# Kernel optimization log

Measured on AMD Instinct MI355X. Metric: run time of the kernel, lower is better.

The kernel has to match this reference:

```python
import jax, jax.numpy as jnp
import numpy as np
from jax import lax

STRIDE, HID, LAT, R, LVL, SCALE = 8, 128, 64, 3, 4, 4
FF = 50 * 60  # frame_flow spatial size


def bilinear_sample(img, x, y):
    # img: [Q,C,H,W]; x,y: [Q,P] float pixel coords; zero outside image. -> [Q,C,P]
    Q, C, H, W = img.shape
    x0 = jnp.floor(x); y0 = jnp.floor(y)
    wx = x - x0; wy = y - y0
    flat = img.reshape(Q, C, H * W)
    def g(ix, iy):
        valid = (ix >= 0) & (ix <= W - 1) & (iy >= 0) & (iy <= H - 1)
        idx = (jnp.clip(iy, 0, H - 1).astype(jnp.int32) * W
               + jnp.clip(ix, 0, W - 1).astype(jnp.int32))[:, None, :]
        v = jnp.take_along_axis(flat, jnp.broadcast_to(idx, (Q, C, x.shape[-1])), axis=2)
        return v * valid[:, None, :]
    return (g(x0, y0) * ((1 - wy) * (1 - wx))[:, None, :]
            + g(x0 + 1, y0) * ((1 - wy) * wx)[:, None, :]
            + g(x0, y0 + 1) * (wy * (1 - wx))[:, None, :]
            + g(x0 + 1, y0 + 1) * (wy * wx)[:, None, :])


def resize_bilinear(img, oh, ow, align_corners):
    # img: [Q,C,H,W] -> [Q,C,oh,ow], matches F.interpolate(mode='bilinear')
    Q, C, H, W = img.shape
    def coords(o, i):
        if align_corners:
            return jnp.linspace(0.0, i - 1.0, o)
        return jnp.clip((jnp.arange(o) + 0.5) * (i / o) - 0.5, 0.0, i - 1.0)
    ys, xs = coords(oh, H), coords(ow, W)
    y0 = jnp.floor(ys).astype(jnp.int32); y1 = jnp.minimum(y0 + 1, H - 1); wy = ys - y0
    x0 = jnp.floor(xs).astype(jnp.int32); x1 = jnp.minimum(x0 + 1, W - 1); wx = xs - x0
    v = jnp.take(img, y0, axis=2) * (1 - wy)[:, None] + jnp.take(img, y1, axis=2) * wy[:, None]
    return jnp.take(v, x0, axis=3) * (1 - wx) + jnp.take(v, x1, axis=3) * wx


def avg_pool2(x):
    return lax.reduce_window(x, 0.0, lax.add, (1, 1, 2, 2), (1, 1, 2, 2), 'VALID') * 0.25


def encode(x, w, stride):
    # patchify conv + instance-norm (surrogate for BasicEncoder, same in/out shapes)
    y = lax.conv_general_dilated(x, w, (stride, stride), 'VALID',
                                 dimension_numbers=('NCHW', 'OIHW', 'NCHW'))
    m = y.mean(axis=(2, 3), keepdims=True)
    v = y.var(axis=(2, 3), keepdims=True)
    return (y - m) * lax.rsqrt(v + 1e-5)


def build_pyramid(fmaps):
    # fmaps: [B,S,C,H,W] -> list of [B*S,C,Hl,Wl] (CorrBlock.__init__)
    B, S, C, H, W = fmaps.shape
    x = fmaps.reshape(B * S, C, H, W)
    pyr = [x]
    for _ in range(LVL - 1):
        x = avg_pool2(x)
        pyr.append(x)
    return pyr


def corr_pyramid(pyr, feats):
    # feats: [B,S,N,C] -> list of [B*S,N,Hl,Wl] (CorrBlock.corr)
    B, S, N, C = feats.shape
    f = feats.reshape(B * S, N, C)
    scale = 1.0 / jnp.sqrt(jnp.float32(C))
    return [jnp.einsum('qnc,qchw->qnhw', f, p) * scale for p in pyr]


def corr_sample(corrs, coords):
    # CorrBlock.sample: bilinear gather of (2R+1)^2 window per level at coords/2^lvl
    B, S, N, _ = coords.shape
    d = jnp.arange(-R, R + 1, dtype=coords.dtype)
    dy, dx = jnp.meshgrid(d, d, indexing='ij')
    dx = dx.reshape(1, -1); dy = dy.reshape(1, -1)
    out = []
    for i, c in enumerate(corrs):
        H, W = c.shape[-2:]
        cen = coords.reshape(B * S * N, 1, 2) / (2.0 ** i)
        x = cen[..., 0] + dx; y = cen[..., 1] + dy  # [BSN,K]
        v = bilinear_sample(c.reshape(B * S * N, 1, H, W), x, y)
        out.append(v.reshape(B, S, N, -1))
    return jnp.concatenate(out, axis=-1)  # [B,S,N,LVL*(2R+1)^2]


def flows_from(coords):
    B, S, N, _ = coords.shape
    f = (coords[:, 1:] - coords[:, :-1]).transpose(0, 2, 1, 3).reshape(B * N, S - 1, 2)
    return jnp.concatenate([f, f[:, -1:]], axis=1)


def delta_block(fc, fl, ff, xy, w1, b1, w2, b2):
    # surrogate for DeltaBlock / DeltaBlock_temp: MLP over concatenated context
    h = jnp.concatenate([fc, fl, ff, xy], axis=-1)
    return jax.nn.relu(h @ w1 + b1) @ w2 + b2  # [B*N,S,2]


def forward_model(rgbs, points_0, fnet_w, fnet_fine_w, linear_w, linear_b,
                  dbs_w1, dbs_b1, dbs_w2, dbs_b2,
                  dbt_w1, dbt_b1, dbt_w2, dbt_b2, iters):
    B, S, C, H, W = rgbs.shape
    N = points_0.shape[1]
    rgbs = 2.0 * (rgbs / 255.0) - 1.0
    rgbs_ = rgbs.reshape(B * S, C, H, W)
    # frame_flow context (assumes B==1, like the torch code): [N,S,3000]
    ff = jnp.concatenate([rgbs_[-1:, 0], rgbs_[1:, 0] - rgbs_[:-1, 0]], axis=0)[:, None]
    ff = resize_bilinear(ff, 50, 60, False).reshape(1, S, FF)
    frame_flow = jnp.broadcast_to(ff, (N, S, FF))

    # ---- initialize_ : coarse stage (stride 8) ----
    Hc, Wc = H // STRIDE, W // STRIDE
    fmaps_c = encode(rgbs_, fnet_w, STRIDE).reshape(B, S, LAT, Hc, Wc)
    coords = jnp.broadcast_to((points_0 / float(STRIDE))[:, None], (B, S, N, 2))
    f0 = bilinear_sample(fmaps_c[:, 0], coords[:, 0, :, 0], coords[:, 0, :, 1]).transpose(0, 2, 1)
    feats = jnp.broadcast_to(f0[:, None], (B, S, N, LAT))
    xys0_c = jnp.broadcast_to(coords[:, 0].transpose(1, 0, 2), (N, S, 2))
    coords = lax.stop_gradient(coords)
    corrs_c = corr_pyramid(build_pyramid(fmaps_c), feats)
    fc = [resize_bilinear(c, 14, 14, True).reshape(B, S, N, 196) for c in corrs_c]
    fcorrs_ = jnp.stack(fc).mean(0).transpose(0, 2, 1, 3).reshape(B * N, S, 196)
    delta = delta_block(fcorrs_, flows_from(coords), frame_flow, xys0_c,
                        dbs_w1, dbs_b1, dbs_w2, dbs_b2)
    coords = coords + delta.reshape(B, N, S, 2).transpose(0, 2, 1, 3)
    coords_init = coords * float(STRIDE)

    # ---- fine refinement (stride 2), iterative ----
    fs = STRIDE // SCALE  # 2
    Hf, Wf = H // fs, W // fs
    fmaps = encode(rgbs_, fnet_fine_w, fs).reshape(B, S, LAT, Hf, Wf)
    coords = coords_init / float(fs)
    pyr = build_pyramid(fmaps)
    f0 = bilinear_sample(fmaps[:, 0], coords[:, 0, :, 0], coords[:, 0, :, 1]).transpose(0, 2, 1)
    corrs1 = corr_pyramid(pyr, jnp.broadcast_to(f0[:, None], (B, S, N, LAT)))
    xys0 = jnp.broadcast_to(coords[:, 0].transpose(1, 0, 2), (N, S, 2))
    inds2 = jnp.clip(jnp.arange(S) - 2, 0, None)
    inds4 = jnp.clip(jnp.arange(S) - 4, 0, None)
    preds = [coords_init]
    for _ in range(iters):
        coords = lax.stop_gradient(coords)
        def shifted_feats(inds, coords=coords):
            fm = fmaps[:, inds].reshape(B * S, LAT, Hf, Wf)
            co = coords[:, inds].reshape(B * S, N, 2)
            return bilinear_sample(fm, co[..., 0], co[..., 1]).transpose(0, 2, 1).reshape(B, S, N, LAT)
        corrs2 = corr_pyramid(pyr, shifted_feats(inds2))
        corrs4 = corr_pyramid(pyr, shifted_feats(inds4))
        def bn(f):
            return f.transpose(0, 2, 1, 3).reshape(B * N, S, -1)
        fcorrs_ = jnp.concatenate([bn(corr_sample(corrs1, coords)),
                                   bn(corr_sample(corrs2, coords)),
                                   bn(corr_sample(corrs4, coords))], axis=2)
        fcorrs_ = fcorrs_ @ linear_w + linear_b  # 588 -> 392
        delta = delta_block(fcorrs_, flows_from(coords), frame_flow, xys0,
                            dbt_w1, dbt_b1, dbt_w2, dbt_b2)
        coords = coords + delta.reshape(B, N, S, 2).transpose(0, 2, 1, 3)
        preds.append(coords * float(fs))
    return jnp.stack(preds)  # [iters+1, B, S, N, 2]


def setup_inputs():
    ks = jax.random.split(jax.random.key(0), 12)
    B, S, N, H, W = 1, 16, 64, 200, 240
    rgbs = jax.random.uniform(ks[0], (B, S, 1, H, W), jnp.float32) * 255.0
    points_0 = jax.random.uniform(ks[1], (B, N, 2), jnp.float32) * jnp.array([W - 1.0, H - 1.0], jnp.float32)
    d_sp, d_tp = 196 + 2 + FF + 2, 392 + 2 + FF + 2
    return {
        'rgbs': rgbs, 'points_0': points_0,
        'fnet_w': jax.random.normal(ks[2], (LAT, 1, STRIDE, STRIDE), jnp.float32) * 0.1,
        'fnet_fine_w': jax.random.normal(ks[3], (LAT, 1, 2, 2), jnp.float32) * 0.3,
        'linear_w': jax.random.normal(ks[4], (588, 392), jnp.float32) / np.sqrt(588.0).astype(np.float32),
        'linear_b': jnp.zeros((392,), jnp.float32),
        'dbs_w1': jax.random.normal(ks[5], (d_sp, HID), jnp.float32) / np.float32(np.sqrt(d_sp)),
        'dbs_b1': jnp.zeros((HID,), jnp.float32),
        'dbs_w2': jax.random.normal(ks[6], (HID, 2), jnp.float32) / np.float32(np.sqrt(HID)),
        'dbs_b2': jnp.zeros((2,), jnp.float32),
        'dbt_w1': jax.random.normal(ks[7], (d_tp, HID), jnp.float32) / np.float32(np.sqrt(d_tp)),
        'dbt_b1': jnp.zeros((HID,), jnp.float32),
        'dbt_w2': jax.random.normal(ks[8], (HID, 2), jnp.float32) / np.float32(np.sqrt(HID)),
        'dbt_b2': jnp.zeros((2,), jnp.float32),
        'iters': 4,
    }


def reference(rgbs, points_0, fnet_w, fnet_fine_w, linear_w, linear_b,
              dbs_w1, dbs_b1, dbs_w2, dbs_b2,
              dbt_w1, dbt_b1, dbt_w2, dbt_b2, iters):
    return forward_model(rgbs, points_0, fnet_w, fnet_fine_w, linear_w, linear_b,
                         dbs_w1, dbs_b1, dbs_w2, dbs_b2,
                         dbt_w1, dbt_b1, dbt_w2, dbt_b2, iters)
```

## Files before the change

kernel.cpp:

```cpp
#include <hip/hip_runtime.h>

constexpr int cS = 16, cN = 64, cH = 200, cW = 240;
constexpr int cHC = 25, cWC = 30;
constexpr int cHF = 100, cWF = 120;
constexpr int cC = 64;
constexpr int cITERS = 4;
constexpr int cNCH = 50, cCHUNK = 60;

typedef _Float16 half8 __attribute__((ext_vector_type(8)));
typedef _Float16 h2 __attribute__((ext_vector_type(2)));


__device__ __forceinline__ float bilin_raw_h(const _Float16* __restrict__ fm, int Hh, int Ww,
                                             float x, float y, int c, float& wsum) {
  x = fminf(fmaxf(x, -2.0e6f), 2.0e6f);
  y = fminf(fmaxf(y, -2.0e6f), 2.0e6f);
  float x0f = floorf(x), y0f = floorf(y);
  int ix = (int)x0f, iy = (int)y0f;
  float wx = x - x0f, wy = y - y0f;
  float acc = 0.f; wsum = 0.f;
  bool vx0 = (ix >= 0) && (ix < Ww), vx1 = (ix + 1 >= 0) && (ix + 1 < Ww);
  bool vy0 = (iy >= 0) && (iy < Hh), vy1 = (iy + 1 >= 0) && (iy + 1 < Hh);
  float w00 = (1.f - wy) * (1.f - wx), w01 = (1.f - wy) * wx;
  float w10 = wy * (1.f - wx), w11 = wy * wx;
  if (vy0 && vx0) { acc += (float)fm[(iy * Ww + ix) * cC + c] * w00; wsum += w00; }
  if (vy0 && vx1) { acc += (float)fm[(iy * Ww + ix + 1) * cC + c] * w01; wsum += w01; }
  if (vy1 && vx0) { acc += (float)fm[((iy + 1) * Ww + ix) * cC + c] * w10; wsum += w10; }
  if (vy1 && vx1) { acc += (float)fm[((iy + 1) * Ww + ix + 1) * cC + c] * w11; wsum += w11; }
  return acc;
}

constexpr int NB_FFP = 800, NB_CONVC = 400, NB_CONVF = 1600;

__global__ __launch_bounds__(256) void k_front(const float* __restrict__ rgbs,
                                               const float* __restrict__ w1s,
                                               const float* __restrict__ w1t,
                                               const float* __restrict__ fnw,
                                               const float* __restrict__ fnfw,
                                               float* __restrict__ part,
                                               _Float16* __restrict__ fmc,
                                               float* __restrict__ partc,
                                               _Float16* __restrict__ fmf,
                                               float* __restrict__ partf) {
  __shared__ float smem[6528];
  int bid = blockIdx.x, tid = threadIdx.x;
  const float a = 2.0f / 255.0f;

  if (bid < NB_FFP) {
    int s = bid / cNCH, ch = bid % cNCH;
    if (tid < cCHUNK) {
      const float* cur = rgbs + (size_t)s * cH * cW;
      const float* prev = rgbs + (size_t)(s - 1) * cH * cW;
      const float* last = rgbs + (size_t)15 * cH * cW;
      int y = 4 * ch + 1, x = 4 * tid + 1;
      float v = 0.f;
      #pragma unroll
      for (int dy = 0; dy < 2; dy++)
        #pragma unroll
        for (int dx = 0; dx < 2; dx++) {
          int id = (y + dy) * cW + (x + dx);
          float pv = (s == 0) ? (a * last[id] - 1.0f) : (a * (cur[id] - prev[id]));
          v += pv;
        }
      smem[tid] = 0.25f * v;
    }
    __syncthreads();
    int t = tid >> 7, j = tid & 127;
    const float* w = (t == 0) ? (w1s + (size_t)198 * 128) : (w1t + (size_t)394 * 128);
    const float* wr = w + (size_t)ch * cCHUNK * 128 + j;
    float acc = 0.f;
    #pragma unroll 4
    for (int i = 0; i < cCHUNK; i++) acc += smem[i] * wr[(size_t)i * 128];
    part[(((size_t)t * cS + s) * cNCH + ch) * 128 + j] = acc;

  } else if (bid < NB_FFP + NB_CONVC) {
    int idx = bid - NB_FFP;
    int q = idx / 25, y = idx % 25;
    float* imgL = smem;
    float* wlT = smem + 1920;
    float* red = smem + 6016;
    const float* img = rgbs + ((size_t)q * cH + y * 8) * cW;
    for (int i = tid; i < 1920; i += 256) imgL[i] = img[i];
    for (int i = tid; i < 4096; i += 256) {
      int tap = i >> 6, c = i & 63;
      wlT[i] = fnw[c * 64 + tap];
    }
    __syncthreads();
    int c = tid & 63, g = tid >> 6;
    float wsum = 0.f;
    for (int t = 0; t < 64; t++) wsum += wlT[t * 64 + c];
    float sum = 0.f, ss = 0.f;
    for (int x = g; x < 30; x += 4) {
      float acc = 0.f;
      #pragma unroll
      for (int ky = 0; ky < 8; ky++)
        #pragma unroll
        for (int kx = 0; kx < 8; kx++)
          acc += wlT[(ky * 8 + kx) * 64 + c] * imgL[ky * 240 + x * 8 + kx];
      float v = a * acc - wsum;
      fmc[((size_t)q * 750 + y * 30 + x) * cC + c] = (_Float16)v;
      sum += v; ss += v * v;
    }
    red[(0 * 4 + g) * 64 + c] = sum;
    red[(1 * 4 + g) * 64 + c] = ss;
    __syncthreads();
    if (g == 0) {
      float s4 = red[0 * 64 + c] + red[1 * 64 + c] + red[2 * 64 + c] + red[3 * 64 + c];
      float q4 = red[(4 + 0) * 64 + c] + red[(4 + 1) * 64 + c] +
                 red[(4 + 2) * 64 + c] + red[(4 + 3) * 64 + c];
      size_t o = ((size_t)q * 25 + y) * 64 + c;
      partc[o * 2 + 0] = s4;
      partc[o * 2 + 1] = q4;
    }

  } else {
    int idx = bid - NB_FFP - NB_CONVC;
    int q = idx / cHF, y = idx % cHF;
    int lane = tid & 63, wv = tid >> 6;
    float w0 = fnfw[lane * 4 + 0], w1 = fnfw[lane * 4 + 1];
    float w2 = fnfw[lane * 4 + 2], w3 = fnfw[lane * 4 + 3];
    float wsum = w0 + w1 + w2 + w3;
    const float* img = rgbs + (size_t)q * cH * cW;
    float sum = 0.f, ss = 0.f;
    for (int x = wv; x < cWF; x += 4) {
      const float* b = img + (2 * y) * cW + 2 * x;
      float v = a * (w0 * b[0] + w1 * b[1] + w2 * b[cW] + w3 * b[cW + 1]) - wsum;
      fmf[(((size_t)q * cHF + y) * cWF + x) * cC + lane] = (_Float16)v;
      sum += v; ss += v * v;
    }
    float* red = smem;
    red[(0 * 4 + wv) * 64 + lane] = sum;
    red[(1 * 4 + wv) * 64 + lane] = ss;
    __syncthreads();
    if (wv == 0) {
      float s4 = red[0 * 64 + lane] + red[1 * 64 + lane] + red[2 * 64 + lane] + red[3 * 64 + lane];
      float q4 = red[(4 + 0) * 64 + lane] + red[(4 + 1) * 64 + lane] +
                 red[(4 + 2) * 64 + lane] + red[(4 + 3) * 64 + lane];
      size_t o = ((size_t)q * cHF + y) * 64 + lane;
      partf[o * 2 + 0] = s4;
      partf[o * 2 + 1] = q4;
    }
  }
}

__global__ __launch_bounds__(256) void k_mid(const float* __restrict__ part,
                                             float* __restrict__ ffw_s, float* __restrict__ ffw_t,
                                             const float* __restrict__ lw, const float* __restrict__ lb,
                                             const float* __restrict__ w1t, const float* __restrict__ b1t,
                                             h2* __restrict__ LWc2, float* __restrict__ b1te,
                                             const float* __restrict__ partf, float* __restrict__ stats,
                                             const float* __restrict__ partc, float* __restrict__ statc,
                                             const _Float16* __restrict__ fmc, float* __restrict__ arp) {
  __shared__ float smem[14784];
  int bid = blockIdx.x, tid = threadIdx.x;

  if (bid < 16) {
    int s = bid, t = tid >> 7, j = tid & 127;
    const float* p = part + (((size_t)t * cS + s) * cNCH) * 128 + j;
    float acc = 0.f;
    for (int c = 0; c < cNCH; c++) acc += p[(size_t)c * 128];
    ((t == 0) ? ffw_s : ffw_t)[s * 128 + j] = acc;

  } else if (bid < 91) {
    int b2 = bid - 16, g = tid >> 7, j = tid & 127;
    if (b2 < 74) {
      int k0 = b2 * 8 + g * 4;
      if (k0 < 588) {
        const float* l0 = lw + (size_t)(k0 + 0) * 392;
        const float* l1 = lw + (size_t)(k0 + 1) * 392;
        const float* l2 = lw + (size_t)(k0 + 2) * 392;
        const float* l3 = lw + (size_t)(k0 + 3) * 392;
        float a0 = 0.f, a1 = 0.f, a2 = 0.f, a3 = 0.f;
        for (int m = 0; m < 392; m++) {
          float wv = w1t[(size_t)m * 128 + j];
          a0 += l0[m] * wv; a1 += l1[m] * wv; a2 += l2[m] * wv; a3 += l3[m] * wv;
        }
        int kk = k0 >> 1;
        LWc2[(size_t)(kk + 0) * 128 + j] = h2{(_Float16)a0, (_Float16)a1};
        LWc2[(size_t)(kk + 1) * 128 + j] = h2{(_Float16)a2, (_Float16)a3};
      }
    } else if (g == 0) {
      float acc = b1t[j];
      for (int m = 0; m < 392; m++) acc += lb[m] * w1t[(size_t)m * 128 + j];
      b1te[j] = acc;
    }

  } else if (bid < 107) {
    int q = bid - 91, c = tid & 63, g = tid >> 6;
    float s0 = 0.f, s1 = 0.f;
    for (int yy = 0; yy < 25; yy++) {
      size_t o = ((size_t)q * cHF + g * 25 + yy) * 64 + c;
      s0 += partf[o * 2 + 0];
      s1 += partf[o * 2 + 1];
    }
    smem[g * 64 + c] = s0;
    smem[256 + g * 64 + c] = s1;
    __syncthreads();
    if (g == 0) {
      stats[(q * 64 + c) * 2 + 0] = smem[c] + smem[64 + c] + smem[128 + c] + smem[192 + c];
      stats[(q * 64 + c) * 2 + 1] = smem[256 + c] + smem[320 + c] + smem[384 + c] + smem[448 + c];
    }

  } else if (bid < 123) {
    int q = bid - 107, c = tid & 63, g = tid >> 6;
    float s0 = 0.f, s1 = 0.f;
    for (int yy = g; yy < 25; yy += 4) {
      size_t o = ((size_t)q * 25 + yy) * 64 + c;
      s0 += partc[o * 2 + 0];
      s1 += partc[o * 2 + 1];
    }
    smem[g * 64 + c] = s0;
    smem[256 + g * 64 + c] = s1;
    __syncthreads();
    if (g == 0) {
      statc[(q * 64 + c) * 2 + 0] = smem[c] + smem[64 + c] + smem[128 + c] + smem[192 + c];
      statc[(q * 64 + c) * 2 + 1] = smem[256 + c] + smem[320 + c] + smem[384 + c] + smem[448 + c];
    }

  } else {
    int q = bid - 123;
    float* pc1 = smem;
    float* pc2 = smem + 11520;
    float* pc3 = smem + 14208;
    const _Float16* L0 = fmc + (size_t)q * 750 * cC;
    for (int i = tid; i < 12 * 15 * 64; i += 256) {
      int c = i & 63, pos = i >> 6, oy = pos / 15, ox = pos % 15;
      const _Float16* b = L0 + ((2 * oy) * 30 + 2 * ox) * cC + c;
      pc1[i] = 0.25f * ((float)b[0] + (float)b[cC] + (float)b[30 * cC] + (float)b[30 * cC + cC]);
    }
    __syncthreads();
    for (int i = tid; i < 6 * 7 * 64; i += 256) {
      int c = i & 63, pos = i >> 6, oy = pos / 7, ox = pos % 7;
      const float* b = pc1 + ((2 * oy) * 15 + 2 * ox) * cC + c;
      pc2[i] = 0.25f * (b[0] + b[cC] + b[15 * cC] + b[15 * cC + cC]);
    }
    __syncthreads();
    for (int i = tid; i < 3 * 3 * 64; i += 256) {
      int c = i & 63, pos = i >> 6, oy = pos / 3, ox = pos % 3;
      const float* b = pc2 + ((2 * oy) * 7 + 2 * ox) * cC + c;
      pc3[i] = 0.25f * (b[0] + b[cC] + b[7 * cC] + b[7 * cC + cC]);
    }
    __syncthreads();
    const int Hs[4] = {25, 12, 6, 3}, Ws[4] = {30, 15, 7, 3};
    for (int i = tid; i < 196 * 64; i += 256) {
      int c = i & 63, pos = i >> 6, o = pos / 14, p = pos % 14;
      float acc = 0.f;
      #pragma unroll
      for (int l = 0; l < 4; l++) {
        float yy = (float)(o * (Hs[l] - 1)) / 13.0f;
        float xx = (float)(p * (Ws[l] - 1)) / 13.0f;
        int y0 = (int)floorf(yy); int y1 = min(y0 + 1, Hs[l] - 1); float wy = yy - (float)y0;
        int x0 = (int)floorf(xx); int x1 = min(x0 + 1, Ws[l] - 1); float wx = xx - (float)x0;
        float v00, v01, v10, v11;
        if (l == 0) {
          v00 = (float)L0[(y0 * 30 + x0) * cC + c]; v01 = (float)L0[(y0 * 30 + x1) * cC + c];
          v10 = (float)L0[(y1 * 30 + x0) * cC + c]; v11 = (float)L0[(y1 * 30 + x1) * cC + c];
        } else {
          const float* L = (l == 1) ? pc1 : ((l == 2) ? pc2 : pc3);
          int Wl = Ws[l];
          v00 = L[(y0 * Wl + x0) * cC + c]; v01 = L[(y0 * Wl + x1) * cC + c];
          v10 = L[(y1 * Wl + x0) * cC + c]; v11 = L[(y1 * Wl + x1) * cC + c];
        }
        acc += (v00 * (1.f - wy) + v10 * wy) * (1.f - wx) + (v01 * (1.f - wy) + v11 * wy) * wx;
      }
      arp[((size_t)q * 196 + pos) * cC + c] = acc * 0.25f * 0.125f;
    }
  }
}

__global__ __launch_bounds__(256) void k_mix(const float* __restrict__ arp, const _Float16* __restrict__ fmc,
                                             const float* __restrict__ statc,
                                             const float* __restrict__ w1, const float* __restrict__ b1,
                                             const float* __restrict__ ffw, const float* __restrict__ w2,
                                             const float* __restrict__ b2, const float* __restrict__ pts,
                                             float* __restrict__ cof, float* __restrict__ xys,
                                             float* __restrict__ out,
                                             const _Float16* __restrict__ fmf,
                                             _Float16* __restrict__ pf1, _Float16* __restrict__ pf2,
                                             _Float16* __restrict__ pf3) {
  __shared__ __align__(16) unsigned char smemraw[38400];
  int bid = blockIdx.x, tid = threadIdx.x;

  if (bid < 256) {
    int n = bid >> 2, sb = (bid & 3) * 4;
    float* fc = (float*)smemraw;
    float* f0n = fc + 784;
    float* featc = f0n + 64;
    float* biasc = featc + 256;
    float* hp = biasc + 4;
    float* hl = hp + 1024;
    float xx = pts[n * 2 + 0] * 0.125f, yy = pts[n * 2 + 1] * 0.125f;
    if (tid < 64) {
      float ws;
      float raw = bilin_raw_h(fmc, cHC, cWC, xx, yy, tid, ws);
      float mu = statc[tid * 2 + 0] / 750.f;
      float var = statc[tid * 2 + 1] / 750.f - mu * mu;
      float r0 = rsqrtf(var + 1e-5f);
      f0n[tid] = r0 * (raw - mu * ws);
    }
    __syncthreads();
    {
      int rr = tid >> 6, c = tid & 63;
      int s = sb + rr;
      float mu = statc[(s * 64 + c) * 2 + 0] / 750.f;
      float var = statc[(s * 64 + c) * 2 + 1] / 750.f - mu * mu;
      float rs = rsqrtf(var + 1e-5f);
      float fv = rs * f0n[c];
      featc[rr * 64 + c] = fv;
      float bc = -0.25f * 0.125f * mu * fv;
      #pragma unroll
      for (int o = 32; o; o >>= 1) bc += __shfl_xor(bc, o);
      if (c == 0) biasc[rr] = bc;
    }
    __syncthreads();
    for (int i = tid; i < 784; i += 256) {
      int r = i / 196, k = i - r * 196;
      const float4* b4 = (const float4*)(arp + ((size_t)(sb + r) * 196 + k) * cC);
      const float* fv = featc + r * 64;
      float acc = 0.f;
      #pragma unroll
      for (int c4 = 0; c4 < 16; c4++) {
        float4 v = b4[c4];
        acc += v.x * fv[c4 * 4 + 0] + v.y * fv[c4 * 4 + 1] +
               v.z * fv[c4 * 4 + 2] + v.w * fv[c4 * 4 + 3];
      }
      fc[i] = acc + biasc[r];
    }
    __syncthreads();
    int j = tid & 127, half = tid >> 7;
    float h0 = 0.f, h1 = 0.f, h2v = 0.f, h3 = 0.f;
    int k0 = half * 98;
    for (int k = k0; k < k0 + 98; k++) {
      float wv = w1[(size_t)k * 128 + j];
      h0 += fc[0 * 196 + k] * wv; h1 += fc[1 * 196 + k] * wv;
      h2v += fc[2 * 196 + k] * wv; h3 += fc[3 * 196 + k] * wv;
    }
    hp[(half * 4 + 0) * 128 + j] = h0; hp[(half * 4 + 1) * 128 + j] = h1;
    hp[(half * 4 + 2) * 128 + j] = h2v; hp[(half * 4 + 3) * 128 + j] = h3;
    __syncthreads();
    if (half == 0) {
      const float* Wxy = w1 + (size_t)3198 * 128;
      #pragma unroll
      for (int r = 0; r < 4; r++) {
        int s = sb + r;
        float v = hp[r * 128 + j] + hp[(4 + r) * 128 + j] + b1[j] +
                  ffw[s * 128 + j] + xx * Wxy[j] + yy * Wxy[128 + j];
        hl[r * 128 + j] = fmaxf(v, 0.f);
      }
    }
    __syncthreads();
    if (tid < 8) {
      int r = tid >> 1, d = tid & 1;
      float acc = b2[d];
      for (int k = 0; k < 128; k++) acc += hl[r * 128 + k] * w2[k * 2 + d];
      int s = sb + r;
      float cc = pts[n * 2 + d] * 0.125f + acc;
      out[((size_t)s * cN + n) * 2 + d] = cc * 8.0f;
      cof[((size_t)s * cN + n) * 2 + d] = cc * 4.0f;
      if (s == 0) xys[n * 2 + d] = cc * 4.0f;
    }

  } else {
    int u = bid - 256;
    int q = u / 13, b = u % 13;
    _Float16* l1 = (_Float16*)smemraw;
    _Float16* l2 = l1 + 15360;
    int nr1 = (b == 12) ? 2 : 4;
    const _Float16* F = fmf + (size_t)q * cHF * cWF * cC;
    for (int i = tid; i < nr1 * 60 * 64; i += 256) {
      int c = i & 63, pos = i >> 6, rl = pos / 60, ox = pos % 60;
      int r1 = 4 * b + rl;
      const _Float16* p = F + ((size_t)(2 * r1) * cWF + 2 * ox) * cC + c;
      float v = 0.25f * ((float)p[0] + (float)p[cC] + (float)p[cWF * cC] + (float)p[cWF * cC + cC]);
      _Float16 h = (_Float16)v;
      l1[i] = h;
      pf1[(((size_t)q * 50 + r1) * 60 + ox) * cC + c] = h;
    }
    __syncthreads();
    int nr2 = (b == 12) ? 1 : 2;
    for (int i = tid; i < nr2 * 30 * 64; i += 256) {
      int c = i & 63, pos = i >> 6, rl = pos / 30, ox = pos % 30;
      const _Float16* p = l1 + ((2 * rl) * 60 + 2 * ox) * 64 + c;
      float v = 0.25f * ((float)p[0] + (float)p[64] + (float)p[60 * 64] + (float)p[60 * 64 + 64]);
      _Float16 h = (_Float16)v;
      l2[i] = h;
      pf2[(((size_t)q * 25 + 2 * b + rl) * 30 + ox) * cC + c] = h;
    }
    __syncthreads();
    if (b < 12) {
      for (int i = tid; i < 15 * 64; i += 256) {
        int c = i & 63, ox = i >> 6;
        const _Float16* p = l2 + (2 * ox) * 64 + c;
        float v = 0.25f * ((float)p[0] + (float)p[64] + (float)p[30 * 64] + (float)p[30 * 64 + 64]);
        pf3[(((size_t)q * 12 + b) * 15 + ox) * cC + c] = (_Float16)v;
      }
    }
  }
}

__global__ __launch_bounds__(256) void k_iter(const _Float16* __restrict__ p0, const _Float16* __restrict__ p1,
                                              const _Float16* __restrict__ p2, const _Float16* __restrict__ p3,
                                              const float* __restrict__ stats,
                                              const h2* __restrict__ LWc2, const float* __restrict__ b1e,
                                              const float* __restrict__ ffw, const float* __restrict__ w1t,
                                              const float* __restrict__ w2, const float* __restrict__ b2,
                                              const float* __restrict__ cof_cur, float* __restrict__ cof_nxt,
                                              const float* __restrict__ xys, float* __restrict__ out) {
  int bid = blockIdx.x;
  int w = (bid & 7) * 128 + (bid >> 3);
  int s = w >> 6, n = w & 63;
  __shared__ _Float16 feat2h[3][64];
  __shared__ float biasS[3];
  __shared__ _Float16 fcL16[588];
  __shared__ float hp[2][128];
  __shared__ float hl[128];
  int tid = threadIdx.x;

  {
    int t = tid >> 6, c = tid & 63;
    if (t < 3) {
      float sS = stats[(s * 64 + c) * 2 + 0], qS = stats[(s * 64 + c) * 2 + 1];
      float meanS = sS / 12000.f, varS = qS / 12000.f - meanS * meanS;
      float rstdS = rsqrtf(varS + 1e-5f);
      int ssrc = (t == 0) ? 0 : max(s - 2 * t, 0);
      float fx, fy;
      if (t == 0) { fx = xys[n * 2 + 0]; fy = xys[n * 2 + 1]; }
      else {
        fx = cof_cur[((size_t)ssrc * cN + n) * 2 + 0];
        fy = cof_cur[((size_t)ssrc * cN + n) * 2 + 1];
      }
      float s2 = stats[(ssrc * 64 + c) * 2 + 0], q2 = stats[(ssrc * 64 + c) * 2 + 1];
      float m2 = s2 / 12000.f, v2 = q2 / 12000.f - m2 * m2;
      float r2 = rsqrtf(v2 + 1e-5f);
      float ws;
      float raw = bilin_raw_h(p0 + (size_t)ssrc * cHF * cWF * cC, cHF, cWF, fx, fy, c, ws);
      float featn = (raw - m2 * ws) * r2;
      feat2h[t][c] = (_Float16)(featn * rstdS * 0.125f);
      float bc = featn * (-meanS * rstdS) * 0.125f;
      #pragma unroll
      for (int o = 32; o; o >>= 1) bc += __shfl_xor(bc, o);
      if (c == 0) biasS[t] = bc;
    }
  }
  __syncthreads();

  {
    int l = tid >> 6, lane = tid & 63;
    const _Float16* Ls[4] = {p0, p1, p2, p3};
    const int Hs[4] = {cHF, 50, 25, 12}, Ws[4] = {cWF, 60, 30, 15};
    const h2* fh0 = (const h2*)feat2h[0];
    const h2* fh1 = (const h2*)feat2h[1];
    const h2* fh2 = (const h2*)feat2h[2];
    float cx = cof_cur[((size_t)s * cN + n) * 2 + 0];
    float cy = cof_cur[((size_t)s * cN + n) * 2 + 1];
    float sc = 1.0f / (float)(1 << l);
    float x = fminf(fmaxf(cx * sc, -2.0e6f), 2.0e6f);
    float y = fminf(fmaxf(cy * sc, -2.0e6f), 2.0e6f);
    float x0f = floorf(x), y0f = floorf(y);
    float wx = x - x0f, wy = y - y0f;
    int dxi = lane & 7, dyi = lane >> 3;
    int ix = (int)x0f + dxi - 3, iy = (int)y0f + dyi - 3;
    int Hl = Hs[l], Wl = Ws[l];
    float d[3] = {0.f, 0.f, 0.f};
    if (ix >= 0 && ix < Wl && iy >= 0 && iy < Hl) {
      const _Float16* row = Ls[l] + (((size_t)s * Hl + iy) * Wl + ix) * cC;
      float a0 = 0.f, a1 = 0.f, a2 = 0.f;
      #pragma unroll
      for (int c8 = 0; c8 < 8; c8++) {
        half8 v = *(const half8*)(row + c8 * 8);
        #pragma unroll
        for (int e2 = 0; e2 < 4; e2++) {
          h2 pv = {v[e2 * 2], v[e2 * 2 + 1]};
          a0 = __builtin_amdgcn_fdot2(pv, fh0[c8 * 4 + e2], a0, false);
          a1 = __builtin_amdgcn_fdot2(pv, fh1[c8 * 4 + e2], a1, false);
          a2 = __builtin_amdgcn_fdot2(pv, fh2[c8 * 4 + e2], a2, false);
        }
      }
      d[0] = a0 + biasS[0]; d[1] = a1 + biasS[1]; d[2] = a2 + biasS[2];
    }
    int dy = lane / 7, dx = lane - dy * 7;
    int bb = (lane < 49) ? (dy * 8 + dx) : 0;
    float w00 = (1.f - wy) * (1.f - wx), w01 = (1.f - wy) * wx;
    float w10 = wy * (1.f - wx), w11 = wy * wx;
    #pragma unroll
    for (int t = 0; t < 3; t++) {
      float d00 = __shfl(d[t], bb, 64);
      float d01 = __shfl(d[t], bb + 1, 64);
      float d10 = __shfl(d[t], bb + 8, 64);
      float d11 = __shfl(d[t], bb + 9, 64);
      if (lane < 49)
        fcL16[t * 196 + l * 49 + lane] = (_Float16)(w00 * d00 + w01 * d01 + w10 * d10 + w11 * d11);
    }
  }
  __syncthreads();

  int j = tid & 127, half = tid >> 7;
  {
    const h2* fcl2 = (const h2*)fcL16;
    float h = 0.f;
    int kk0 = half * 147;
    const h2* Lw = LWc2 + (size_t)kk0 * 128 + j;
    #pragma unroll 4
    for (int kk = 0; kk < 147; kk++)
      h = __builtin_amdgcn_fdot2(fcl2[kk0 + kk], Lw[(size_t)kk * 128], h, false);
    hp[half][j] = h;
  }
  __syncthreads();
  if (half == 0) {
    const float* Wfl = w1t + (size_t)392 * 128;
    const float* Wxy = w1t + (size_t)3394 * 128;
    float xx = xys[n * 2 + 0], yy = xys[n * 2 + 1];
    int sA = min(s + 1, 15), sB = (s == 15) ? 14 : s;
    float flx = cof_cur[(sA * cN + n) * 2 + 0] - cof_cur[(sB * cN + n) * 2 + 0];
    float fly = cof_cur[(sA * cN + n) * 2 + 1] - cof_cur[(sB * cN + n) * 2 + 1];
    float v = hp[0][j] + hp[1][j] + b1e[j] + ffw[s * 128 + j] +
              flx * Wfl[j] + fly * Wfl[128 + j] + xx * Wxy[j] + yy * Wxy[128 + j];
    hl[j] = fmaxf(v, 0.f);
  }
  __syncthreads();
  if (tid < 2) {
    int d = tid;
    float acc = b2[d];
    for (int k = 0; k < 128; k++) acc += hl[k] * w2[k * 2 + d];
    float cc = cof_cur[((size_t)s * cN + n) * 2 + d] + acc;
    cof_nxt[((size_t)s * cN + n) * 2 + d] = cc;
    out[((size_t)s * cN + n) * 2 + d] = cc * 2.0f;
  }
}

extern "C" void kernel_launch(void* const* d_in, const int* in_sizes, int n_in,
                              void* d_out, int out_size, void* d_ws, size_t ws_size,
                              hipStream_t stream) {
  (void)in_sizes; (void)n_in; (void)out_size; (void)ws_size;
  const float* rgbs = (const float*)d_in[0];
  const float* pts  = (const float*)d_in[1];
  const float* fnw  = (const float*)d_in[2];
  const float* fnfw = (const float*)d_in[3];
  const float* lw   = (const float*)d_in[4];
  const float* lb   = (const float*)d_in[5];
  const float* w1s  = (const float*)d_in[6];
  const float* b1s  = (const float*)d_in[7];
  const float* w2s  = (const float*)d_in[8];
  const float* b2s  = (const float*)d_in[9];
  const float* w1t  = (const float*)d_in[10];
  const float* b1t  = (const float*)d_in[11];
  const float* w2t  = (const float*)d_in[12];
  const float* b2t  = (const float*)d_in[13];
  float* out = (float*)d_out;

  float* p = (float*)d_ws;
  auto alloc = [&](size_t nf) { float* r = p; p += nf; return r; };
  float* part  = alloc((size_t)2 * cS * cNCH * 128);
  float* ffw_s = alloc(cS * 128);
  float* ffw_t = alloc(cS * 128);
  h2* LWc2     = (h2*)alloc((size_t)588 * 128 / 2);
  float* b1te  = alloc(128);
  _Float16* fmc = (_Float16*)alloc((size_t)cS * 750 * cC / 2);
  float* partc = alloc((size_t)cS * 25 * cC * 2);
  float* statc = alloc(cS * cC * 2);
  float* arp   = alloc((size_t)cS * 196 * cC);
  float* partf = alloc((size_t)cS * cHF * cC * 2);
  float* stats = alloc(cS * cC * 2);
  _Float16* fmf = (_Float16*)alloc((size_t)cS * cHF * cWF * cC / 2);
  _Float16* pf1 = (_Float16*)alloc((size_t)cS * 50 * 60 * cC / 2);
  _Float16* pf2 = (_Float16*)alloc((size_t)cS * 25 * 30 * cC / 2);
  _Float16* pf3 = (_Float16*)alloc((size_t)cS * 12 * 15 * cC / 2);
  float* xys0  = alloc(cN * 2);
  float* cofA  = alloc((size_t)cS * cN * 2);
  float* cofB  = alloc((size_t)cS * cN * 2);

  k_front<<<NB_FFP + NB_CONVC + NB_CONVF, 256, 0, stream>>>(
      rgbs, w1s, w1t, fnw, fnfw, part, fmc, partc, fmf, partf);
  k_mid<<<139, 256, 0, stream>>>(part, ffw_s, ffw_t, lw, lb, w1t, b1t, LWc2, b1te,
                                 partf, stats, partc, statc, fmc, arp);
  k_mix<<<464, 256, 0, stream>>>(arp, fmc, statc, w1s, b1s, ffw_s, w2s, b2s, pts,
                                 cofA, xys0, out, fmf, pf1, pf2, pf3);
  float* cbuf[2] = {cofA, cofB};
  for (int it = 0; it < cITERS; it++) {
    float* cur = cbuf[it & 1];
    float* nxt = cbuf[(it & 1) ^ 1];
    k_iter<<<1024, 256, 0, stream>>>(fmf, pf1, pf2, pf3, stats, LWc2, b1te, ffw_t,
                                     w1t, w2t, b2t, cur, nxt, xys0,
                                     out + (size_t)(it + 1) * cS * cN * 2);
  }
}
```

Baseline: 173.0 us.

## Process two time rows per k_iter block and move fine pyramid pooling into k_mid

k_iter now handles two (s, n) pairs per block, with rows s and s+8. This halves the grid and lets each LWc2 weight value loaded in the MLP dot-product feed two accumulators. The fine-pyramid pooling blocks move from k_mix into k_mid, leaving k_mix with only the 256 initial-mix blocks. Per-thread work in the correlation phase doubles, which may lengthen latency chains and lower occupancy in exchange for the weight reuse.

```diff
diff --git a/kernel.cpp b/kernel.cpp
--- a/kernel.cpp
+++ b/kernel.cpp
@@ -150,7 +150,10 @@
                                              h2* __restrict__ LWc2, float* __restrict__ b1te,
                                              const float* __restrict__ partf, float* __restrict__ stats,
                                              const float* __restrict__ partc, float* __restrict__ statc,
-                                             const _Float16* __restrict__ fmc, float* __restrict__ arp) {
+                                             const _Float16* __restrict__ fmc, float* __restrict__ arp,
+                                             const _Float16* __restrict__ fmf,
+                                             _Float16* __restrict__ pf1, _Float16* __restrict__ pf2,
+                                             _Float16* __restrict__ pf3) {
   __shared__ float smem[14784];
   int bid = blockIdx.x, tid = threadIdx.x;
 
@@ -217,7 +220,7 @@
       statc[(q * 64 + c) * 2 + 1] = smem[256 + c] + smem[320 + c] + smem[384 + c] + smem[448 + c];
     }
 
-  } else {
+  } else if (bid < 139) {
     int q = bid - 123;
     float* pc1 = smem;
     float* pc2 = smem + 11520;
@@ -265,105 +268,11 @@
       }
       arp[((size_t)q * 196 + pos) * cC + c] = acc * 0.25f * 0.125f;
     }
-  }
-}
-
-__global__ __launch_bounds__(256) void k_mix(const float* __restrict__ arp, const _Float16* __restrict__ fmc,
-                                             const float* __restrict__ statc,
-                                             const float* __restrict__ w1, const float* __restrict__ b1,
-                                             const float* __restrict__ ffw, const float* __restrict__ w2,
-                                             const float* __restrict__ b2, const float* __restrict__ pts,
-                                             float* __restrict__ cof, float* __restrict__ xys,
-                                             float* __restrict__ out,
-                                             const _Float16* __restrict__ fmf,
-                                             _Float16* __restrict__ pf1, _Float16* __restrict__ pf2,
-                                             _Float16* __restrict__ pf3) {
-  __shared__ __align__(16) unsigned char smemraw[38400];
-  int bid = blockIdx.x, tid = threadIdx.x;
-
-  if (bid < 256) {
-    int n = bid >> 2, sb = (bid & 3) * 4;
-    float* fc = (float*)smemraw;
-    float* f0n = fc + 784;
-    float* featc = f0n + 64;
-    float* biasc = featc + 256;
-    float* hp = biasc + 4;
-    float* hl = hp + 1024;
-    float xx = pts[n * 2 + 0] * 0.125f, yy = pts[n * 2 + 1] * 0.125f;
-    if (tid < 64) {
-      float ws;
-      float raw = bilin_raw_h(fmc, cHC, cWC, xx, yy, tid, ws);
-      float mu = statc[tid * 2 + 0] / 750.f;
-      float var = statc[tid * 2 + 1] / 750.f - mu * mu;
-      float r0 = rsqrtf(var + 1e-5f);
-      f0n[tid] = r0 * (raw - mu * ws);
-    }
-    __syncthreads();
-    {
-      int rr = tid >> 6, c = tid & 63;
-      int s = sb + rr;
-      float mu = statc[(s * 64 + c) * 2 + 0] / 750.f;
-      float var = statc[(s * 64 + c) * 2 + 1] / 750.f - mu * mu;
-      float rs = rsqrtf(var + 1e-5f);
-      float fv = rs * f0n[c];
-      featc[rr * 64 + c] = fv;
-      float bc = -0.25f * 0.125f * mu * fv;
-      #pragma unroll
-      for (int o = 32; o; o >>= 1) bc += __shfl_xor(bc, o);
-      if (c == 0) biasc[rr] = bc;
-    }
-    __syncthreads();
-    for (int i = tid; i < 784; i += 256) {
-      int r = i / 196, k = i - r * 196;
-      const float4* b4 = (const float4*)(arp + ((size_t)(sb + r) * 196 + k) * cC);
-      const float* fv = featc + r * 64;
-      float acc = 0.f;
-      #pragma unroll
-      for (int c4 = 0; c4 < 16; c4++) {
-        float4 v = b4[c4];
-        acc += v.x * fv[c4 * 4 + 0] + v.y * fv[c4 * 4 + 1] +
-               v.z * fv[c4 * 4 + 2] + v.w * fv[c4 * 4 + 3];
-      }
-      fc[i] = acc + biasc[r];
-    }
-    __syncthreads();
-    int j = tid & 127, half = tid >> 7;
-    float h0 = 0.f, h1 = 0.f, h2v = 0.f, h3 = 0.f;
-    int k0 = half * 98;
-    for (int k = k0; k < k0 + 98; k++) {
-      float wv = w1[(size_t)k * 128 + j];
-      h0 += fc[0 * 196 + k] * wv; h1 += fc[1 * 196 + k] * wv;
-      h2v += fc[2 * 196 + k] * wv; h3 += fc[3 * 196 + k] * wv;
-    }
-    hp[(half * 4 + 0) * 128 + j] = h0; hp[(half * 4 + 1) * 128 + j] = h1;
-    hp[(half * 4 + 2) * 128 + j] = h2v; hp[(half * 4 + 3) * 128 + j] = h3;
-    __syncthreads();
-    if (half == 0) {
-      const float* Wxy = w1 + (size_t)3198 * 128;
-      #pragma unroll
-      for (int r = 0; r < 4; r++) {
-        int s = sb + r;
-        float v = hp[r * 128 + j] + hp[(4 + r) * 128 + j] + b1[j] +
-                  ffw[s * 128 + j] + xx * Wxy[j] + yy * Wxy[128 + j];
-        hl[r * 128 + j] = fmaxf(v, 0.f);
-      }
-    }
-    __syncthreads();
-    if (tid < 8) {
-      int r = tid >> 1, d = tid & 1;
-      float acc = b2[d];
-      for (int k = 0; k < 128; k++) acc += hl[r * 128 + k] * w2[k * 2 + d];
-      int s = sb + r;
-      float cc = pts[n * 2 + d] * 0.125f + acc;
-      out[((size_t)s * cN + n) * 2 + d] = cc * 8.0f;
-      cof[((size_t)s * cN + n) * 2 + d] = cc * 4.0f;
-      if (s == 0) xys[n * 2 + d] = cc * 4.0f;
-    }
 
   } else {
-    int u = bid - 256;
+    int u = bid - 139;
     int q = u / 13, b = u % 13;
-    _Float16* l1 = (_Float16*)smemraw;
+    _Float16* l1 = (_Float16*)smem;
     _Float16* l2 = l1 + 15360;
     int nr1 = (b == 12) ? 2 : 4;
     const _Float16* F = fmf + (size_t)q * cHF * cWF * cC;
@@ -398,6 +307,94 @@
   }
 }
 
+__global__ __launch_bounds__(256) void k_mix(const float* __restrict__ arp, const _Float16* __restrict__ fmc,
+                                             const float* __restrict__ statc,
+                                             const float* __restrict__ w1, const float* __restrict__ b1,
+                                             const float* __restrict__ ffw, const float* __restrict__ w2,
+                                             const float* __restrict__ b2, const float* __restrict__ pts,
+                                             float* __restrict__ cof, float* __restrict__ xys,
+                                             float* __restrict__ out) {
+  __shared__ float fc[784];
+  __shared__ float f0n[64];
+  __shared__ float featc[256];
+  __shared__ float biasc[4];
+  __shared__ float hp[1024];
+  __shared__ float hl[512];
+  int bid = blockIdx.x, tid = threadIdx.x;
+
+  int n = bid >> 2, sb = (bid & 3) * 4;
+  float xx = pts[n * 2 + 0] * 0.125f, yy = pts[n * 2 + 1] * 0.125f;
+  if (tid < 64) {
+    float ws;
+    float raw = bilin_raw_h(fmc, cHC, cWC, xx, yy, tid, ws);
+    float mu = statc[tid * 2 + 0] / 750.f;
+    float var = statc[tid * 2 + 1] / 750.f - mu * mu;
+    float r0 = rsqrtf(var + 1e-5f);
+    f0n[tid] = r0 * (raw - mu * ws);
+  }
+  __syncthreads();
+  {
+    int rr = tid >> 6, c = tid & 63;
+    int s = sb + rr;
+    float mu = statc[(s * 64 + c) * 2 + 0] / 750.f;
+    float var = statc[(s * 64 + c) * 2 + 1] / 750.f - mu * mu;
+    float rs = rsqrtf(var + 1e-5f);
+    float fv = rs * f0n[c];
+    featc[rr * 64 + c] = fv;
+    float bc = -0.25f * 0.125f * mu * fv;
+    #pragma unroll
+    for (int o = 32; o; o >>= 1) bc += __shfl_xor(bc, o);
+    if (c == 0) biasc[rr] = bc;
+  }
+  __syncthreads();
+  for (int i = tid; i < 784; i += 256) {
+    int r = i / 196, k = i - r * 196;
+    const float4* b4 = (const float4*)(arp + ((size_t)(sb + r) * 196 + k) * cC);
+    const float* fv = featc + r * 64;
+    float acc = 0.f;
+    #pragma unroll
+    for (int c4 = 0; c4 < 16; c4++) {
+      float4 v = b4[c4];
+      acc += v.x * fv[c4 * 4 + 0] + v.y * fv[c4 * 4 + 1] +
+             v.z * fv[c4 * 4 + 2] + v.w * fv[c4 * 4 + 3];
+    }
+    fc[i] = acc + biasc[r];
+  }
+  __syncthreads();
+  int j = tid & 127, half = tid >> 7;
+  float h0 = 0.f, h1 = 0.f, h2v = 0.f, h3 = 0.f;
+  int k0 = half * 98;
+  for (int k = k0; k < k0 + 98; k++) {
+    float wv = w1[(size_t)k * 128 + j];
+    h0 += fc[0 * 196 + k] * wv; h1 += fc[1 * 196 + k] * wv;
+    h2v += fc[2 * 196 + k] * wv; h3 += fc[3 * 196 + k] * wv;
+  }
+  hp[(half * 4 + 0) * 128 + j] = h0; hp[(half * 4 + 1) * 128 + j] = h1;
+  hp[(half * 4 + 2) * 128 + j] = h2v; hp[(half * 4 + 3) * 128 + j] = h3;
+  __syncthreads();
+  if (half == 0) {
+    const float* Wxy = w1 + (size_t)3198 * 128;
+    #pragma unroll
+    for (int r = 0; r < 4; r++) {
+      int s = sb + r;
+      float v = hp[r * 128 + j] + hp[(4 + r) * 128 + j] + b1[j] +
+                ffw[s * 128 + j] + xx * Wxy[j] + yy * Wxy[128 + j];
+      hl[r * 128 + j] = fmaxf(v, 0.f);
+    }
+  }
+  __syncthreads();
+  if (tid < 8) {
+    int r = tid >> 1, d = tid & 1;
+    float acc = b2[d];
+    for (int k = 0; k < 128; k++) acc += hl[r * 128 + k] * w2[k * 2 + d];
+    int s = sb + r;
+    float cc = pts[n * 2 + d] * 0.125f + acc;
+    out[((size_t)s * cN + n) * 2 + d] = cc * 8.0f;
+    cof[((size_t)s * cN + n) * 2 + d] = cc * 4.0f;
+    if (s == 0) xys[n * 2 + d] = cc * 4.0f;
+  }
+}
+
 __global__ __launch_bounds__(256) void k_iter(const _Float16* __restrict__ p0, const _Float16* __restrict__ p1,
                                               const _Float16* __restrict__ p2, const _Float16* __restrict__ p3,
                                               const float* __restrict__ stats,
@@ -407,39 +404,48 @@
                                               const float* __restrict__ cof_cur, float* __restrict__ cof_nxt,
                                               const float* __restrict__ xys, float* __restrict__ out) {
   int bid = blockIdx.x;
-  int w = (bid & 7) * 128 + (bid >> 3);
-  int s = w >> 6, n = w & 63;
-  __shared__ _Float16 feat2h[3][64];
-  __shared__ float biasS[3];
-  __shared__ _Float16 fcL16[588];
-  __shared__ float hp[2][128];
-  __shared__ float hl[128];
+  int w = (bid & 7) * 64 + (bid >> 3);
+  int n = w & 63;
+  int srow[2] = {w >> 6, (w >> 6) + 8};
+  __shared__ _Float16 feat2h[2][3][64];
+  __shared__ float biasS[2][3];
+  __shared__ _Float16 fcL16[2][588];
+  __shared__ float hp[2][2][128];
+  __shared__ float hl[2][128];
   int tid = threadIdx.x;
 
   {
-    int t = tid >> 6, c = tid & 63;
-    if (t < 3) {
-      float sS = stats[(s * 64 + c) * 2 + 0], qS = stats[(s * 64 + c) * 2 + 1];
-      float meanS = sS / 12000.f, varS = qS / 12000.f - meanS * meanS;
-      float rstdS = rsqrtf(varS + 1e-5f);
-      int ssrc = (t == 0) ? 0 : max(s - 2 * t, 0);
-      float fx, fy;
-      if (t == 0) { fx = xys[n * 2 + 0]; fy = xys[n * 2 + 1]; }
-      else {
-        fx = cof_cur[((size_t)ssrc * cN + n) * 2 + 0];
-        fy = cof_cur[((size_t)ssrc * cN + n) * 2 + 1];
+    int c = tid & 63, wv = tid >> 6;
+    #pragma unroll
+    for (int pass = 0; pass < 2; pass++) {
+      int u = wv + pass * 4;
+      if (u < 6) {
+        int r = u >> 1 >= 3 ? 1 : u / 3;
+        r = u / 3;
+        int t = u - r * 3;
+        int s = srow[r];
+        float sS = stats[(s * 64 + c) * 2 + 0], qS = stats[(s * 64 + c) * 2 + 1];
+        float meanS = sS / 12000.f, varS = qS / 12000.f - meanS * meanS;
+        float rstdS = rsqrtf(varS + 1e-5f);
+        int ssrc = (t == 0) ? 0 : max(s - 2 * t, 0);
+        float fx, fy;
+        if (t == 0) { fx = xys[n * 2 + 0]; fy = xys[n * 2 + 1]; }
+        else {
+          fx = cof_cur[((size_t)ssrc * cN + n) * 2 + 0];
+          fy = cof_cur[((size_t)ssrc * cN + n) * 2 + 1];
+        }
+        float s2 = stats[(ssrc * 64 + c) * 2 + 0], q2 = stats[(ssrc * 64 + c) * 2 + 1];
+        float m2 = s2 / 12000.f, v2 = q2 / 12000.f - m2 * m2;
+        float r2 = rsqrtf(v2 + 1e-5f);
+        float ws;
+        float raw = bilin_raw_h(p0 + (size_t)ssrc * cHF * cWF * cC, cHF, cWF, fx, fy, c, ws);
+        float featn = (raw - m2 * ws) * r2;
+        feat2h[r][t][c] = (_Float16)(featn * rstdS * 0.125f);
+        float bc = featn * (-meanS * rstdS) * 0.125f;
+        #pragma unroll
+        for (int o = 32; o; o >>= 1) bc += __shfl_xor(bc, o);
+        if (c == 0) biasS[r][t] = bc;
       }
-      float s2 = stats[(ssrc * 64 + c) * 2 + 0], q2 = stats[(ssrc * 64 + c) * 2 + 1];
-      float m2 = s2 / 12000.f, v2 = q2 / 12000.f - m2 * m2;
-      float r2 = rsqrtf(v2 + 1e-5f);
-      float ws;
-      float raw = bilin_raw_h(p0 + (size_t)ssrc * cHF * cWF * cC, cHF, cWF, fx, fy, c, ws);
-      float featn = (raw - m2 * ws) * r2;
-      feat2h[t][c] = (_Float16)(featn * rstdS * 0.125f);
-      float bc = featn * (-meanS * rstdS) * 0.125f;
-      #pragma unroll
-      for (int o = 32; o; o >>= 1) bc += __shfl_xor(bc, o);
-      if (c == 0) biasS[t] = bc;
     }
   }
   __syncthreads();
@@ -448,80 +454,92 @@
     int l = tid >> 6, lane = tid & 63;
     const _Float16* Ls[4] = {p0, p1, p2, p3};
     const int Hs[4] = {cHF, 50, 25, 12}, Ws[4] = {cWF, 60, 30, 15};
-    const h2* fh0 = (const h2*)feat2h[0];
-    const h2* fh1 = (const h2*)feat2h[1];
-    const h2* fh2 = (const h2*)feat2h[2];
-    float cx = cof_cur[((size_t)s * cN + n) * 2 + 0];
-    float cy = cof_cur[((size_t)s * cN + n) * 2 + 1];
-    float sc = 1.0f / (float)(1 << l);
-    float x = fminf(fmaxf(cx * sc, -2.0e6f), 2.0e6f);
-    float y = fminf(fmaxf(cy * sc, -2.0e6f), 2.0e6f);
-    float x0f = floorf(x), y0f = floorf(y);
-    float wx = x - x0f, wy = y - y0f;
     int dxi = lane & 7, dyi = lane >> 3;
-    int ix = (int)x0f + dxi - 3, iy = (int)y0f + dyi - 3;
-    int Hl = Hs[l], Wl = Ws[l];
-    float d[3] = {0.f, 0.f, 0.f};
-    if (ix >= 0 && ix < Wl && iy >= 0 && iy < Hl) {
-      const _Float16* row = Ls[l] + (((size_t)s * Hl + iy) * Wl + ix) * cC;
-      float a0 = 0.f, a1 = 0.f, a2 = 0.f;
+    int dy7 = lane / 7, dx7 = lane - dy7 * 7;
+    int bb = (lane < 49) ? (dy7 * 8 + dx7) : 0;
+    #pragma unroll
+    for (int r = 0; r < 2; r++) {
+      int s = srow[r];
+      const h2* fh0 = (const h2*)feat2h[r][0];
+      const h2* fh1 = (const h2*)feat2h[r][1];
+      const h2* fh2 = (const h2*)feat2h[r][2];
+      float cx = cof_cur[((size_t)s * cN + n) * 2 + 0];
+      float cy = cof_cur[((size_t)s * cN + n) * 2 + 1];
+      float sc = 1.0f / (float)(1 << l);
+      float x = fminf(fmaxf(cx * sc, -2.0e6f), 2.0e6f);
+      float y = fminf(fmaxf(cy * sc, -2.0e6f), 2.0e6f);
+      float x0f = floorf(x), y0f = floorf(y);
+      float wx = x - x0f, wy = y - y0f;
+      int ix = (int)x0f + dxi - 3, iy = (int)y0f + dyi - 3;
+      int Hl = Hs[l], Wl = Ws[l];
+      float d[3] = {0.f, 0.f, 0.f};
+      if (ix >= 0 && ix < Wl && iy >= 0 && iy < Hl) {
+        const _Float16* row = Ls[l] + (((size_t)s * Hl + iy) * Wl + ix) * cC;
+        float a0 = 0.f, a1 = 0.f, a2 = 0.f;
+        #pragma unroll
+        for (int c8 = 0; c8 < 8; c8++) {
+          half8 v = *(const half8*)(row + c8 * 8);
+          #pragma unroll
+          for (int e2 = 0; e2 < 4; e2++) {
+            h2 pv = {v[e2 * 2], v[e2 * 2 + 1]};
+            a0 = __builtin_amdgcn_fdot2(pv, fh0[c8 * 4 + e2], a0, false);
+            a1 = __builtin_amdgcn_fdot2(pv, fh1[c8 * 4 + e2], a1, false);
+            a2 = __builtin_amdgcn_fdot2(pv, fh2[c8 * 4 + e2], a2, false);
+          }
+        }
+        d[0] = a0 + biasS[r][0]; d[1] = a1 + biasS[r][1]; d[2] = a2 + biasS[r][2];
+      }
+      float w00 = (1.f - wy) * (1.f - wx), w01 = (1.f - wy) * wx;
+      float w10 = wy * (1.f - wx), w11 = wy * wx;
       #pragma unroll
-      for (int c8 = 0; c8 < 8; c8++) {
-        half8 v = *(const half8*)(row + c8 * 8);
-        #pragma unroll
-        for (int e2 = 0; e2 < 4; e2++) {
-          h2 pv = {v[e2 * 2], v[e2 * 2 + 1]};
-          a0 = __builtin_amdgcn_fdot2(pv, fh0[c8 * 4 + e2], a0, false);
-          a1 = __builtin_amdgcn_fdot2(pv, fh1[c8 * 4 + e2], a1, false);
-          a2 = __builtin_amdgcn_fdot2(pv, fh2[c8 * 4 + e2], a2, false);
-        }
+      for (int t = 0; t < 3; t++) {
+        float d00 = __shfl(d[t], bb, 64);
+        float d01 = __shfl(d[t], bb + 1, 64);
+        float d10 = __shfl(d[t], bb + 8, 64);
+        float d11 = __shfl(d[t], bb + 9, 64);
+        if (lane < 49)
+          fcL16[r][t * 196 + l * 49 + lane] =
+              (_Float16)(w00 * d00 + w01 * d01 + w10 * d10 + w11 * d11);
       }
-      d[0] = a0 + biasS[0]; d[1] = a1 + biasS[1]; d[2] = a2 + biasS[2];
-    }
-    int dy = lane / 7, dx = lane - dy * 7;
-    int bb = (lane < 49) ? (dy * 8 + dx) : 0;
-    float w00 = (1.f - wy) * (1.f - wx), w01 = (1.f - wy) * wx;
-    float w10 = wy * (1.f - wx), w11 = wy * wx;
-    #pragma unroll
-    for (int t = 0; t < 3; t++) {
-      float d00 = __shfl(d[t], bb, 64);
-      float d01 = __shfl(d[t], bb + 1, 64);
-      float d10 = __shfl(d[t], bb + 8, 64);
-      float d11 = __shfl(d[t], bb + 9, 64);
-      if (lane < 49)
-        fcL16[t * 196 + l * 49 + lane] = (_Float16)(w00 * d00 + w01 * d01 + w10 * d10 + w11 * d11);
     }
   }
   __syncthreads();
 
   int j = tid & 127, half = tid >> 7;
   {
-    const h2* fcl2 = (const h2*)fcL16;
-    float h = 0.f;
+    const h2* f0 = (const h2*)fcL16[0];
+    const h2* f1 = (const h2*)fcL16[1];
+    float h0 = 0.f, h1 = 0.f;
     int kk0 = half * 147;
     const h2* Lw = LWc2 + (size_t)kk0 * 128 + j;
     #pragma unroll 4
-    for (int kk = 0; kk < 147; kk++)
-      h = __builtin_amdgcn_fdot2(fcl2[kk0 + kk], Lw[(size_t)kk * 128], h, false);
-    hp[half][j] = h;
-  }
-  __syncthreads();
-  if (half == 0) {
+    for (int kk = 0; kk < 147; kk++) {
+      h2 wv = Lw[(size_t)kk * 128];
+      h0 = __builtin_amdgcn_fdot2(f0[kk0 + kk], wv, h0, false);
+      h1 = __builtin_amdgcn_fdot2(f1[kk0 + kk], wv, h1, false);
+    }
+    hp[half][0][j] = h0; hp[half][1][j] = h1;
+  }
+  __syncthreads();
+  {
+    int r = half;
+    int s = srow[r];
     const float* Wfl = w1t + (size_t)392 * 128;
     const float* Wxy = w1t + (size_t)3394 * 128;
     float xx = xys[n * 2 + 0], yy = xys[n * 2 + 1];
     int sA = min(s + 1, 15), sB = (s == 15) ? 14 : s;
     float flx = cof_cur[(sA * cN + n) * 2 + 0] - cof_cur[(sB * cN + n) * 2 + 0];
     float fly = cof_cur[(sA * cN + n) * 2 + 1] - cof_cur[(sB * cN + n) * 2 + 1];
-    float v = hp[0][j] + hp[1][j] + b1e[j] + ffw[s * 128 + j] +
+    float v = hp[0][r][j] + hp[1][r][j] + b1e[j] + ffw[s * 128 + j] +
               flx * Wfl[j] + fly * Wfl[128 + j] + xx * Wxy[j] + yy * Wxy[128 + j];
-    hl[j] = fmaxf(v, 0.f);
-  }
-  __syncthreads();
-  if (tid < 2) {
-    int d = tid;
+    hl[r][j] = fmaxf(v, 0.f);
+  }
+  __syncthreads();
+  if (tid < 4) {
+    int r = tid >> 1, d = tid & 1;
+    int s = srow[r];
     float acc = b2[d];
-    for (int k = 0; k < 128; k++) acc += hl[k] * w2[k * 2 + d];
+    for (int k = 0; k < 128; k++) acc += hl[r][k] * w2[k * 2 + d];
     float cc = cof_cur[((size_t)s * cN + n) * 2 + d] + acc;
     cof_nxt[((size_t)s * cN + n) * 2 + d] = cc;
     out[((size_t)s * cN + n) * 2 + d] = cc * 2.0f;
@@ -571,16 +589,17 @@
 
   k_front<<<NB_FFP + NB_CONVC + NB_CONVF, 256, 0, stream>>>(
       rgbs, w1s, w1t, fnw, fnfw, part, fmc, partc, fmf, partf);
-  k_mid<<<139, 256, 0, stream>>>(part, ffw_s, ffw_t, lw, lb, w1t, b1t, LWc2, b1te,
-                                 partf, stats, partc, statc, fmc, arp);
-  k_mix<<<464, 256, 0, stream>>>(arp, fmc, statc, w1s, b1s, ffw_s, w2s, b2s, pts,
-                                 cofA, xys0, out, fmf, pf1, pf2, pf3);
+  k_mid<<<347, 256, 0, stream>>>(part, ffw_s, ffw_t, lw, lb, w1t, b1t, LWc2, b1te,
+                                 partf, stats, partc, statc, fmc, arp,
+                                 fmf, pf1, pf2, pf3);
+  k_mix<<<256, 256, 0, stream>>>(arp, fmc, statc, w1s, b1s, ffw_s, w2s, b2s, pts,
+                                 cofA, xys0, out);
   float* cbuf[2] = {cofA, cofB};
   for (int it = 0; it < cITERS; it++) {
     float* cur = cbuf[it & 1];
     float* nxt = cbuf[(it & 1) ^ 1];
-    k_iter<<<1024, 256, 0, stream>>>(fmf, pf1, pf2, pf3, stats, LWc2, b1te, ffw_t,
-                                     w1t, w2t, b2t, cur, nxt, xys0,
-                                     out + (size_t)(it + 1) * cS * cN * 2);
+    k_iter<<<512, 256, 0, stream>>>(fmf, pf1, pf2, pf3, stats, LWc2, b1te, ffw_t,
+                                    w1t, w2t, b2t, cur, nxt, xys0,
+                                    out + (size_t)(it + 1) * cS * cN * 2);
   }
 }
```

Result: slower. 183.9 us (+6.3%).
